# Optimization experiments

Measured on AMD Instinct MI355X. Metric: run time of the kernel, lower is better.

## Reference

```python
import jax, jax.numpy as jnp
import numpy as np

ALPHA = 0.05          # embed strength (frames in [0,1])
COEF_R, COEF_C = 4, 3 # mid-frequency DCT coefficient that carries the bit


def _dct_mat():
    # 8x8 orthonormal DCT-II matrix
    n = jnp.arange(8, dtype=jnp.float32)
    D = jnp.cos(jnp.pi * (2.0 * n[None, :] + 1.0) * n[:, None] / 16.0) * jnp.sqrt(2.0 / 8.0)
    return D.at[0].multiply(1.0 / jnp.sqrt(2.0))


def rgb_to_yuv(rgb):
    r, g, b = rgb[:, 0:1], rgb[:, 1:2], rgb[:, 2:3]
    y = 0.299 * r + 0.587 * g + 0.114 * b
    u = -0.147 * r - 0.289 * g + 0.436 * b
    v = 0.615 * r - 0.515 * g - 0.1 * b
    return jnp.concatenate([y, u, v], axis=1)


def yuv_to_rgb(yuv):
    y, u, v = yuv[:, 0:1], yuv[:, 1:2], yuv[:, 2:3]
    r = y + 1.14 * v
    g = y - 0.395 * u - 0.581 * v
    b = y + 2.032 * u
    return jnp.concatenate([r, g, b], axis=1)


def lbp_uniform(gray):
    # uniform LBP, P=8, R=1 (integer 8-neighborhood), per-image max-normalized
    B, H, W = gray.shape
    p = jnp.pad(gray, ((0, 0), (1, 1), (1, 1)), mode='edge')
    offs = [(-1, 0), (-1, 1), (0, 1), (1, 1), (1, 0), (1, -1), (0, -1), (-1, -1)]
    neigh = jnp.stack([p[:, 1 + dy:1 + dy + H, 1 + dx:1 + dx + W] for dy, dx in offs], axis=0)
    bits = (neigh >= gray[None]).astype(jnp.float32)          # [8,B,H,W]
    trans = jnp.sum(jnp.abs(bits - jnp.roll(bits, 1, axis=0)), axis=0)
    s = jnp.sum(bits, axis=0)
    code = jnp.where(trans <= 2.0, s, 9.0)
    mx = jnp.max(code, axis=(1, 2), keepdims=True)
    return code / mx                                           # [B,H,W]


def dct_embed(y, watermark, mask):
    # y: [B,H,W] luma; watermark: [L] int bits; mask: [B,H,W] texture strength
    B, H, W = y.shape
    nh, nw = H // 8, W // 8
    D = _dct_mat()
    yb = y.reshape(B, nh, 8, nw, 8).transpose(0, 1, 3, 2, 4)   # [B,nh,nw,8,8]
    coef = jnp.einsum('ij,bhwjk,lk->bhwil', D, yb, D)          # D @ block @ D^T
    strength = mask.reshape(B, nh, 8, nw, 8).mean(axis=(2, 4)) # [B,nh,nw]
    L = watermark.shape[0]
    idx = (jnp.arange(nh * nw) % L).reshape(nh, nw)
    bits = watermark[idx].astype(jnp.float32)                  # [nh,nw]
    delta = ALPHA * strength * (2.0 * bits - 1.0)[None]        # [B,nh,nw]
    coef = coef.at[..., COEF_R, COEF_C].add(delta)
    inv = jnp.einsum('ji,bhwjk,kl->bhwil', D, coef, D)         # D^T @ coef @ D
    return inv.transpose(0, 1, 3, 2, 4).reshape(B, H, W)


def _forward(frame, watermark, sa_w, sa_b, ca_w1, ca_w2):
    # LBP texture features from grayscale
    gray = 0.299 * frame[:, 0] + 0.587 * frame[:, 1] + 0.114 * frame[:, 2]
    lbp = lbp_uniform(gray)[:, None]                           # [B,1,H,W]
    # spatial attention: 7x7 conv over [frame, lbp] -> sigmoid mask
    sa_in = jnp.concatenate([frame, lbp], axis=1)
    mask = jax.nn.sigmoid(
        jax.lax.conv_general_dilated(sa_in, sa_w, (1, 1), 'SAME',
                                     dimension_numbers=('NCHW', 'OIHW', 'NCHW'))
        + sa_b[None, :, None, None])                           # [B,1,H,W]
    # channel attention on YUV
    yuv = rgb_to_yuv(frame)
    pooled = yuv.mean(axis=(2, 3))                             # [B,3]
    scale = jax.nn.sigmoid(jax.nn.relu(pooled @ ca_w1.T) @ ca_w2.T)
    weighted = yuv * scale[:, :, None, None]
    # blockwise DCT watermark embed on Y channel
    y_marked = dct_embed(weighted[:, 0], watermark, mask[:, 0])
    wm_yuv = jnp.concatenate([y_marked[:, None], weighted[:, 1:2], weighted[:, 2:3]], axis=1)
    return yuv_to_rgb(wm_yuv), mask


def setup_inputs() -> dict:
    key = jax.random.key(0)
    k1, k2, k3, k4, k5 = jax.random.split(key, 5)
    B, H, W, L = 16, 512, 512, 64
    frame = jax.random.uniform(k1, (B, 3, H, W), dtype=jnp.float32)
    watermark = jax.random.randint(k2, (L,), 0, 2, dtype=jnp.int32)
    sa_w = jax.random.normal(k3, (1, 4, 7, 7), dtype=jnp.float32) * 0.1
    sa_b = jnp.zeros((1,), dtype=jnp.float32)
    ca_w1 = jax.random.normal(k4, (3, 3), dtype=jnp.float32) * 0.5
    ca_w2 = jax.random.normal(k5, (3, 3), dtype=jnp.float32) * 0.5
    return {"frame": frame, "watermark": watermark, "sa_w": sa_w, "sa_b": sa_b,
            "ca_w1": ca_w1, "ca_w2": ca_w2}


def reference(frame, watermark, sa_w, sa_b, ca_w1, ca_w2):
    return _forward(frame, watermark, sa_w, sa_b, ca_w1, ca_w2)
```

## Files before the change

### kernel.cpp

```cpp
#include <hip/hip_runtime.h>
#include <stdint.h>

#define BB 16
#define HH 512
#define WW 512
#define HWsz (HH*WW)

__device__ __forceinline__ float grayf(float r,float g,float b){
  return __fadd_rn(__fadd_rn(__fmul_rn(0.299f,r),__fmul_rn(0.587f,g)),__fmul_rn(0.114f,b));
}
__device__ __forceinline__ float sigmoidf_(float x){ return 1.0f/(1.0f+expf(-x)); }

__device__ __forceinline__ int lbp_code(float tl,float tc,float tr,
                                        float ml,float c ,float mr,
                                        float bl,float bc,float br){
  int b0 = tc>=c, b1 = tr>=c, b2 = mr>=c, b3 = br>=c;
  int b4 = bc>=c, b5 = bl>=c, b6 = ml>=c, b7 = tl>=c;
  int s = (b0+b1)+(b2+b3)+(b4+b5)+(b6+b7);
  int tr_ = (b0!=b7)+(b1!=b0)+(b2!=b1)+(b3!=b2)+(b4!=b3)+(b5!=b4)+(b6!=b5)+(b7!=b6);
  return (tr_<=2)? s : 9;
}

__global__ void k_init(float* sums, int* maxc){
  int t = threadIdx.x;
  if(t < BB*3) sums[t] = 0.0f;
  if(t < BB) maxc[t] = 0;
}

#define RSTRIDE 520
__global__ __launch_bounds__(256,4) void k_reduce(const float* __restrict__ frame,
     float* __restrict__ sums, int* __restrict__ maxc){
  const int blk = blockIdx.x;
  const int b = blk >> 6;
  const int s = blk & 63;
  const int r0 = s*8;
  const float4* F = (const float4*)(frame + (size_t)b*3*HWsz);
  __shared__ float sg[10*RSTRIDE];
  const int tid = threadIdx.x;
  float sy=0.f, su=0.f, sv=0.f;
  #pragma unroll
  for(int k=0;k<5;k++){
    int j = tid + 256*k;
    int row = j >> 7;
    int c4  = j & 127;
    int gy  = min(max(r0-1+row,0),HH-1);
    int fi  = gy*128 + c4;
    float4 r4 = F[fi];
    float4 g4 = F[65536  + fi];
    float4 b4 = F[131072 + fi];
    float4 gr;
    gr.x = grayf(r4.x,g4.x,b4.x);
    gr.y = grayf(r4.y,g4.y,b4.y);
    gr.z = grayf(r4.z,g4.z,b4.z);
    gr.w = grayf(r4.w,g4.w,b4.w);
    *(float4*)&sg[row*RSTRIDE + 4 + 4*c4] = gr;
    if(c4==0)   sg[row*RSTRIDE + 3]   = gr.x;
    if(c4==127) sg[row*RSTRIDE + 516] = gr.w;
    if(row>=1 && row<=8){
      sy += (gr.x+gr.y)+(gr.z+gr.w);
      float rs_=(r4.x+r4.y)+(r4.z+r4.w), gs_=(g4.x+g4.y)+(g4.z+g4.w), bs_=(b4.x+b4.y)+(b4.z+b4.w);
      su += -0.147f*rs_ - 0.289f*gs_ + 0.436f*bs_;
      sv +=  0.615f*rs_ - 0.515f*gs_ - 0.1f*bs_;
    }
  }
  __syncthreads();
  int cm = 0;
  {
    const float* base = sg + (2*tid + 3);
    float t0=base[0], t1=base[1], t2=base[2], t3=base[3];
    float m0=base[RSTRIDE], m1=base[RSTRIDE+1], m2=base[RSTRIDE+2], m3=base[RSTRIDE+3];
    #pragma unroll
    for(int R=1;R<=8;R++){
      const float* brow = base + (R+1)*RSTRIDE;
      float b0=brow[0], b1=brow[1], b2=brow[2], b3=brow[3];
      cm = max(cm, lbp_code(t0,t1,t2, m0,m1,m2, b0,b1,b2));
      cm = max(cm, lbp_code(t1,t2,t3, m1,m2,m3, b1,b2,b3));
      t0=m0;t1=m1;t2=m2;t3=m3; m0=b0;m1=b1;m2=b2;m3=b3;
    }
  }
  #pragma unroll
  for(int off=32;off>=1;off>>=1){
    sy += __shfl_down(sy,off,64);
    su += __shfl_down(su,off,64);
    sv += __shfl_down(sv,off,64);
    cm = max(cm,__shfl_down(cm,off,64));
  }
  __shared__ float rs[3][4]; __shared__ int rm[4];
  int wave=tid>>6, lane=tid&63;
  if(lane==0){ rs[0][wave]=sy; rs[1][wave]=su; rs[2][wave]=sv; rm[wave]=cm; }
  __syncthreads();
  if(tid==0){
    atomicAdd(&sums[b*3+0], (rs[0][0]+rs[0][1])+(rs[0][2]+rs[0][3]));
    atomicAdd(&sums[b*3+1], (rs[1][0]+rs[1][1])+(rs[1][2]+rs[1][3]));
    atomicAdd(&sums[b*3+2], (rs[2][0]+rs[2][1])+(rs[2][2]+rs[2][3]));
    atomicMax(&maxc[b], max(max(rm[0],rm[1]),max(rm[2],rm[3])));
  }
}

__global__ void k_scale(const float* __restrict__ sums, const int* __restrict__ maxc,
    const float* __restrict__ w1, const float* __restrict__ w2,
    float* __restrict__ scale, float* __restrict__ mxf){
  int b = threadIdx.x;
  if(b >= BB) return;
  float p[3], h[3];
  for(int j=0;j<3;j++) p[j] = sums[b*3+j] * (1.0f/(float)HWsz);
  for(int i=0;i<3;i++){
    float a = p[0]*w1[i*3+0] + p[1]*w1[i*3+1] + p[2]*w1[i*3+2];
    h[i] = fmaxf(a, 0.0f);
  }
  for(int i=0;i<3;i++){
    float a = h[0]*w2[i*3+0] + h[1]*w2[i*3+1] + h[2]*w2[i*3+2];
    scale[b*3+i] = sigmoidf_(a);
  }
  mxf[b] = fmaxf((float)maxc[b], 1.0f);
}

#define SAS 41
__global__ __launch_bounds__(256,6) void k_main(const float* __restrict__ frame,
    const int* __restrict__ wm, const float* __restrict__ sa_w, const float* __restrict__ sa_b,
    const float* __restrict__ scalev, const float* __restrict__ mxf,
    float* __restrict__ out)
{
  const int b = blockIdx.z;
  const int tx0 = blockIdx.x*32, ty0 = blockIdx.y*32;
  const float* fr = frame + (size_t)b*3*HWsz;
  const float4* F4 = (const float4*)fr;

  __shared__ float sA[4][38][SAS];
  __shared__ float sgt[44];
  __shared__ float sgb[44];
  __shared__ float spart[32][8];
  __shared__ float sstr[4][4];
  __shared__ float ssc[4];
  __shared__ float scodetab[12];

  const int tid = threadIdx.x;
  if(tid < 3)  ssc[tid] = scalev[b*3 + tid];
  if(tid == 3) ssc[3] = sa_b[0];
  if(tid < 10) scodetab[tid] = (float)tid / mxf[b];

  for(int s = tid; s < 400; s += 256){
    int ly = s / 10;
    int k  = s - ly*10;
    int gy = ty0 + ly - 4;
    int ry = min(max(gy,0),HH-1);
    int gx0 = tx0 + 4*k - 4;
    bool xin = (gx0 >= 0) && (gx0 <= WW-4);
    float4 r4, g4, b4;
    if(xin){
      int fi = ry*(WW/4) + (gx0>>2);
      r4 = F4[fi]; g4 = F4[65536 + fi]; b4 = F4[131072 + fi];
    } else {
      int cc = (gx0 < 0) ? 0 : (WW-1);
      float r = fr[ry*WW+cc], g = fr[HWsz+ry*WW+cc], bl = fr[2*HWsz+ry*WW+cc];
      r4 = make_float4(r,r,r,r); g4 = make_float4(g,g,g,g); b4 = make_float4(bl,bl,bl,bl);
    }
    float gr0 = grayf(r4.x,g4.x,b4.x), gr1 = grayf(r4.y,g4.y,b4.y),
          gr2 = grayf(r4.z,g4.z,b4.z), gr3 = grayf(r4.w,g4.w,b4.w);
    int cbase = 4*k;
    float* gp = (ly==0) ? &sgt[cbase] : ((ly==39) ? &sgb[cbase] : &sA[3][ly-1][cbase]);
    gp[0]=gr0; gp[1]=gr1; gp[2]=gr2; gp[3]=gr3;
    if(ly >= 1 && ly <= 38){
      float z = ((gy >= 0) && (gy < HH) && xin) ? 1.0f : 0.0f;
      float* rp = &sA[0][ly-1][cbase];
      rp[0]          =r4.x*z; rp[1]          =r4.y*z; rp[2]          =r4.z*z; rp[3]          =r4.w*z;
      rp[38*SAS+0]   =g4.x*z; rp[38*SAS+1]   =g4.y*z; rp[38*SAS+2]   =g4.z*z; rp[38*SAS+3]   =g4.w*z;
      rp[2*38*SAS+0] =b4.x*z; rp[2*38*SAS+1] =b4.y*z; rp[2*38*SAS+2] =b4.z*z; rp[2*38*SAS+3] =b4.w*z;
    }
  }
  __syncthreads();

  float lv[2][4];
  #pragma unroll
  for(int it=0; it<2; ++it){
    int s2 = tid + 256*it;
    if(s2 < 380){
      int lr = s2 / 10;
      int q  = s2 - lr*10;
      int lx0 = 4*q;
      const float* rowM = &sA[3][lr][0];
      const float* rowT = (lr==0)  ? sgt : &sA[3][lr-1][0];
      const float* rowB = (lr==37) ? sgb : &sA[3][lr+1][0];
      float t_[6], m_[6], b_[6];
      #pragma unroll
      for(int j=0;j<6;j++){
        int c = lx0 - 1 + j;
        t_[j]=rowT[c]; m_[j]=rowM[c]; b_[j]=rowB[c];
      }
      int gy = ty0 + lr - 3;
      bool rowin = (gy >= 0) && (gy < HH);
      #pragma unroll
      for(int j=0;j<4;j++){
        int lx = lx0 + j;
        int gx = tx0 + lx - 4;
        float v = 0.0f;
        if(rowin && lx >= 1 && lx <= 38 && gx >= 0 && gx < WW){
          float c = m_[j+1];
          int msk = ((t_[j+1]>=c)?1:0)   | ((t_[j+2]>=c)?2:0)  | ((m_[j+2]>=c)?4:0) |
                    ((b_[j+2]>=c)?8:0)   | ((b_[j+1]>=c)?16:0) | ((b_[j]>=c)?32:0)  |
                    ((m_[j]>=c)?64:0)    | ((t_[j]>=c)?128:0);
          int s8  = __popc(msk);
          int rot = ((msk<<1) | (msk>>7)) & 255;
          int tr_ = __popc(msk ^ rot);
          int code = (tr_ <= 2) ? s8 : 9;
          v = scodetab[code];
        }
        lv[it][j] = v;
      }
    }
  }
  __syncthreads();
  #pragma unroll
  for(int it=0; it<2; ++it){
    int s2 = tid + 256*it;
    if(s2 < 380){
      int lr = s2 / 10;
      int q  = s2 - lr*10;
      float* wp2 = &sA[3][lr][4*q];
      wp2[0]=lv[it][0]; wp2[1]=lv[it][1]; wp2[2]=lv[it][2]; wp2[3]=lv[it][3];
    }
  }
  __syncthreads();

  const int t  = tid & 7;
  const int ty = tid >> 3;
  float a0=ssc[3], a1=ssc[3], a2=ssc[3], a3=ssc[3];
  for(int ci=0;ci<4;ci++){
    #pragma unroll
    for(int ky=0;ky<7;ky++){
      const float* rowp = &sA[ci][ty+ky][4*t];
      float win[10];
      #pragma unroll
      for(int w=0;w<10;w++) win[w]=rowp[1+w];
      const float* wr = &sa_w[ci*49 + ky*7];
      #pragma unroll
      for(int kx=0;kx<7;kx++){
        float wt = wr[kx];
        a0 += win[kx+0]*wt;
        a1 += win[kx+1]*wt;
        a2 += win[kx+2]*wt;
        a3 += win[kx+3]*wt;
      }
    }
  }
  float m0=sigmoidf_(a0), m1=sigmoidf_(a1), m2=sigmoidf_(a2), m3=sigmoidf_(a3);
  {
    size_t midx = (size_t)(3*BB)*HWsz + (size_t)b*HWsz + (size_t)(ty0+ty)*WW + (size_t)(tx0+4*t);
    *reinterpret_cast<float4*>(out + midx) = make_float4(m0,m1,m2,m3);
  }
  spart[ty][t] = (m0+m1)+(m2+m3);
  __syncthreads();

  if(tid<16){
    int rb=tid>>2, cb=tid&3;
    float ssum=0.f;
    #pragma unroll
    for(int yy=0;yy<8;yy++) ssum += spart[rb*8+yy][2*cb] + spart[rb*8+yy][2*cb+1];
    sstr[rb][cb]=ssum*(1.0f/64.0f);
  }
  __syncthreads();

  {
    const float sc0=ssc[0], sc1=ssc[1], sc2=ssc[2];
    const float strength = sstr[ty>>3][t>>1];
    const int bw = (tx0 + 4*t) >> 3;
    const float sgn = (float)(2*wm[bw]-1);
    const float d4 = (((ty+1)&2) ? -0.35355339059327373f : 0.35355339059327373f);
    const float delta = 0.05f * strength * sgn * d4;
    const float D3tab[8] = { 0.4157348061512726f,-0.0975451610080641f,-0.4903926402016152f,-0.2777851165098011f,
                             0.2777851165098011f, 0.4903926402016152f, 0.0975451610080641f,-0.4157348061512726f };
    float vr[4], vg[4], vb[4];
    #pragma unroll
    for(int j=0;j<4;j++){
      float r  = sA[0][ty+3][4*t+j+4];
      float g  = sA[1][ty+3][4*t+j+4];
      float bl = sA[2][ty+3][4*t+j+4];
      float yv = (0.299f*r + 0.587f*g + 0.114f*bl) * sc0;
      float uv = (-0.147f*r - 0.289f*g + 0.436f*bl) * sc1;
      float vv = ( 0.615f*r - 0.515f*g - 0.1f*bl) * sc2;
      float ym = yv + delta * D3tab[(t&1)*4 + j];
      vr[j] = ym + 1.14f*vv;
      vg[j] = ym - 0.395f*uv - 0.581f*vv;
      vb[j] = ym + 2.032f*uv;
    }
    size_t base = (size_t)(ty0+ty)*WW + (size_t)(tx0+4*t);
    *reinterpret_cast<float4*>(out + (size_t)(b*3+0)*HWsz + base) = make_float4(vr[0],vr[1],vr[2],vr[3]);
    *reinterpret_cast<float4*>(out + (size_t)(b*3+1)*HWsz + base) = make_float4(vg[0],vg[1],vg[2],vg[3]);
    *reinterpret_cast<float4*>(out + (size_t)(b*3+2)*HWsz + base) = make_float4(vb[0],vb[1],vb[2],vb[3]);
  }
}

extern "C" void kernel_launch(void* const* d_in, const int* in_sizes, int n_in,
                              void* d_out, int out_size, void* d_ws, size_t ws_size,
                              hipStream_t stream) {
  const float* frame = (const float*)d_in[0];
  const int*   wmark = (const int*)d_in[1];
  const float* sa_w  = (const float*)d_in[2];
  const float* sa_b  = (const float*)d_in[3];
  const float* ca_w1 = (const float*)d_in[4];
  const float* ca_w2 = (const float*)d_in[5];
  float* out = (float*)d_out;
  char* ws = (char*)d_ws;
  float* sums  = (float*)(ws);
  int*   maxc  = (int*)(ws + 192);
  float* scalev= (float*)(ws + 256);
  float* mxf   = (float*)(ws + 448);

  hipLaunchKernelGGL(k_init,  dim3(1),        dim3(64),  0, stream, sums, maxc);
  hipLaunchKernelGGL(k_reduce,dim3(1024),     dim3(256), 0, stream, frame, sums, maxc);
  hipLaunchKernelGGL(k_scale, dim3(1),        dim3(64),  0, stream, sums, maxc, ca_w1, ca_w2, scalev, mxf);
  hipLaunchKernelGGL(k_main,  dim3(16,16,16), dim3(256), 0, stream, frame, wmark, sa_w, sa_b, scalev, mxf, out);
}
```

Measured before the change: 174.7 us.

## Widen main tile to 64 columns with 8 outputs per thread and shuffle-reduce strength

Doubles the k_main tile width to 64 columns, so each thread computes eight horizontal outputs of the 7x7 attention conv and the watermark. This cuts halo reload overhead and amortises shared-memory window loads over more outputs. Each thread now covers exactly one 8-wide DCT block column, so the per-block mean strength is computed with wavefront xor-shuffles instead of a shared-memory partial array and two barriers. The trade-off is more registers and shared memory per block, with launch bounds lowered from 6 to 3 blocks per CU, which reduces occupancy.

```diff
diff --git a/kernel.cpp b/kernel.cpp
--- a/kernel.cpp
+++ b/kernel.cpp
@@ -115,22 +115,20 @@
   mxf[b] = fmaxf((float)maxc[b], 1.0f);
 }
 
-#define SAS 41
-__global__ __launch_bounds__(256,6) void k_main(const float* __restrict__ frame,
+#define SAS 73
+__global__ __launch_bounds__(256,3) void k_main(const float* __restrict__ frame,
     const int* __restrict__ wm, const float* __restrict__ sa_w, const float* __restrict__ sa_b,
     const float* __restrict__ scalev, const float* __restrict__ mxf,
     float* __restrict__ out)
 {
   const int b = blockIdx.z;
-  const int tx0 = blockIdx.x*32, ty0 = blockIdx.y*32;
+  const int tx0 = blockIdx.x*64, ty0 = blockIdx.y*32;
   const float* fr = frame + (size_t)b*3*HWsz;
   const float4* F4 = (const float4*)fr;
 
   __shared__ float sA[4][38][SAS];
-  __shared__ float sgt[44];
-  __shared__ float sgb[44];
-  __shared__ float spart[32][8];
-  __shared__ float sstr[4][4];
+  __shared__ float sgt[76];
+  __shared__ float sgb[76];
   __shared__ float ssc[4];
   __shared__ float scodetab[12];
 
@@ -139,9 +137,9 @@
   if(tid == 3) ssc[3] = sa_b[0];
   if(tid < 10) scodetab[tid] = (float)tid / mxf[b];
 
-  for(int s = tid; s < 400; s += 256){
-    int ly = s / 10;
-    int k  = s - ly*10;
+  for(int s = tid; s < 720; s += 256){
+    int ly = s / 18;
+    int k  = s - ly*18;
     int gy = ty0 + ly - 4;
     int ry = min(max(gy,0),HH-1);
     int gx0 = tx0 + 4*k - 4;
@@ -170,13 +168,13 @@
   }
   __syncthreads();
 
-  float lv[2][4];
+  float lv[3][4];
   #pragma unroll
-  for(int it=0; it<2; ++it){
+  for(int it=0; it<3; ++it){
     int s2 = tid + 256*it;
-    if(s2 < 380){
-      int lr = s2 / 10;
-      int q  = s2 - lr*10;
+    if(s2 < 684){
+      int lr = s2 / 18;
+      int q  = s2 - lr*18;
       int lx0 = 4*q;
       const float* rowM = &sA[3][lr][0];
       const float* rowT = (lr==0)  ? sgt : &sA[3][lr-1][0];
@@ -194,7 +192,7 @@
         int lx = lx0 + j;
         int gx = tx0 + lx - 4;
         float v = 0.0f;
-        if(rowin && lx >= 1 && lx <= 38 && gx >= 0 && gx < WW){
+        if(rowin && lx >= 1 && lx <= 70 && gx >= 0 && gx < WW){
           float c = m_[j+1];
           int msk = ((t_[j+1]>=c)?1:0)   | ((t_[j+2]>=c)?2:0)  | ((m_[j+2]>=c)?4:0) |
                     ((b_[j+2]>=c)?8:0)   | ((b_[j+1]>=c)?16:0) | ((b_[j]>=c)?32:0)  |
@@ -211,11 +209,11 @@
   }
   __syncthreads();
   #pragma unroll
-  for(int it=0; it<2; ++it){
+  for(int it=0; it<3; ++it){
     int s2 = tid + 256*it;
-    if(s2 < 380){
-      int lr = s2 / 10;
-      int q  = s2 - lr*10;
+    if(s2 < 684){
+      int lr = s2 / 18;
+      int q  = s2 - lr*18;
       float* wp2 = &sA[3][lr][4*q];
       wp2[0]=lv[it][0]; wp2[1]=lv[it][1]; wp2[2]=lv[it][2]; wp2[3]=lv[it][3];
     }
@@ -225,13 +223,14 @@
   const int t  = tid & 7;
   const int ty = tid >> 3;
   float a0=ssc[3], a1=ssc[3], a2=ssc[3], a3=ssc[3];
+  float a4=ssc[3], a5=ssc[3], a6=ssc[3], a7=ssc[3];
   for(int ci=0;ci<4;ci++){
     #pragma unroll
     for(int ky=0;ky<7;ky++){
-      const float* rowp = &sA[ci][ty+ky][4*t];
-      float win[10];
+      const float* rowp = &sA[ci][ty+ky][8*t];
+      float win[14];
       #pragma unroll
-      for(int w=0;w<10;w++) win[w]=rowp[1+w];
+      for(int w=0;w<14;w++) win[w]=rowp[1+w];
       const float* wr = &sa_w[ci*49 + ky*7];
       #pragma unroll
       for(int kx=0;kx<7;kx++){
@@ -240,53 +239,60 @@
         a1 += win[kx+1]*wt;
         a2 += win[kx+2]*wt;
         a3 += win[kx+3]*wt;
+        a4 += win[kx+4]*wt;
+        a5 += win[kx+5]*wt;
+        a6 += win[kx+6]*wt;
+        a7 += win[kx+7]*wt;
       }
     }
   }
-  float m0=sigmoidf_(a0), m1=sigmoidf_(a1), m2=sigmoidf_(a2), m3=sigmoidf_(a3);
+  float m[8];
+  m[0]=sigmoidf_(a0); m[1]=sigmoidf_(a1); m[2]=sigmoidf_(a2); m[3]=sigmoidf_(a3);
+  m[4]=sigmoidf_(a4); m[5]=sigmoidf_(a5); m[6]=sigmoidf_(a6); m[7]=sigmoidf_(a7);
   {
-    size_t midx = (size_t)(3*BB)*HWsz + (size_t)b*HWsz + (size_t)(ty0+ty)*WW + (size_t)(tx0+4*t);
-    *reinterpret_cast<float4*>(out + midx) = make_float4(m0,m1,m2,m3);
-  }
-  spart[ty][t] = (m0+m1)+(m2+m3);
-  __syncthreads();
-
-  if(tid<16){
-    int rb=tid>>2, cb=tid&3;
-    float ssum=0.f;
-    #pragma unroll
-    for(int yy=0;yy<8;yy++) ssum += spart[rb*8+yy][2*cb] + spart[rb*8+yy][2*cb+1];
-    sstr[rb][cb]=ssum*(1.0f/64.0f);
-  }
-  __syncthreads();
+    size_t midx = (size_t)(3*BB)*HWsz + (size_t)b*HWsz + (size_t)(ty0+ty)*WW + (size_t)(tx0+8*t);
+    *reinterpret_cast<float4*>(out + midx)     = make_float4(m[0],m[1],m[2],m[3]);
+    *reinterpret_cast<float4*>(out + midx + 4) = make_float4(m[4],m[5],m[6],m[7]);
+  }
+
+  float part = ((m[0]+m[1])+(m[2]+m[3])) + ((m[4]+m[5])+(m[6]+m[7]));
+  part += __shfl_xor(part, 8, 64);
+  part += __shfl_xor(part, 16, 64);
+  part += __shfl_xor(part, 32, 64);
+  const float strength = part * (1.0f/64.0f);
 
   {
     const float sc0=ssc[0], sc1=ssc[1], sc2=ssc[2];
-    const float strength = sstr[ty>>3][t>>1];
-    const int bw = (tx0 + 4*t) >> 3;
+    const int bw = (tx0 + 8*t) >> 3;
     const float sgn = (float)(2*wm[bw]-1);
     const float d4 = (((ty+1)&2) ? -0.35355339059327373f : 0.35355339059327373f);
     const float delta = 0.05f * strength * sgn * d4;
     const float D3tab[8] = { 0.4157348061512726f,-0.0975451610080641f,-0.4903926402016152f,-0.2777851165098011f,
                              0.2777851165098011f, 0.4903926402016152f, 0.0975451610080641f,-0.4157348061512726f };
-    float vr[4], vg[4], vb[4];
+    float vr[8], vg[8], vb[8];
     #pragma unroll
-    for(int j=0;j<4;j++){
-      float r  = sA[0][ty+3][4*t+j+4];
-      float g  = sA[1][ty+3][4*t+j+4];
-      float bl = sA[2][ty+3][4*t+j+4];
+    for(int j=0;j<8;j++){
+      float r  = sA[0][ty+3][8*t+j+4];
+      float g  = sA[1][ty+3][8*t+j+4];
+      float bl = sA[2][ty+3][8*t+j+4];
       float yv = (0.299f*r + 0.587f*g + 0.114f*bl) * sc0;
       float uv = (-0.147f*r - 0.289f*g + 0.436f*bl) * sc1;
       float vv = ( 0.615f*r - 0.515f*g - 0.1f*bl) * sc2;
-      float ym = yv + delta * D3tab[(t&1)*4 + j];
+      float ym = yv + delta * D3tab[j];
       vr[j] = ym + 1.14f*vv;
       vg[j] = ym - 0.395f*uv - 0.581f*vv;
       vb[j] = ym + 2.032f*uv;
     }
-    size_t base = (size_t)(ty0+ty)*WW + (size_t)(tx0+4*t);
-    *reinterpret_cast<float4*>(out + (size_t)(b*3+0)*HWsz + base) = make_float4(vr[0],vr[1],vr[2],vr[3]);
-    *reinterpret_cast<float4*>(out + (size_t)(b*3+1)*HWsz + base) = make_float4(vg[0],vg[1],vg[2],vg[3]);
-    *reinterpret_cast<float4*>(out + (size_t)(b*3+2)*HWsz + base) = make_float4(vb[0],vb[1],vb[2],vb[3]);
+    size_t base = (size_t)(ty0+ty)*WW + (size_t)(tx0+8*t);
+    float* o0 = out + (size_t)(b*3+0)*HWsz + base;
+    float* o1 = out + (size_t)(b*3+1)*HWsz + base;
+    float* o2 = out + (size_t)(b*3+2)*HWsz + base;
+    *reinterpret_cast<float4*>(o0)   = make_float4(vr[0],vr[1],vr[2],vr[3]);
+    *reinterpret_cast<float4*>(o0+4) = make_float4(vr[4],vr[5],vr[6],vr[7]);
+    *reinterpret_cast<float4*>(o1)   = make_float4(vg[0],vg[1],vg[2],vg[3]);
+    *reinterpret_cast<float4*>(o1+4) = make_float4(vg[4],vg[5],vg[6],vg[7]);
+    *reinterpret_cast<float4*>(o2)   = make_float4(vb[0],vb[1],vb[2],vb[3]);
+    *reinterpret_cast<float4*>(o2+4) = make_float4(vb[4],vb[5],vb[6],vb[7]);
   }
 }
 
@@ -309,5 +315,5 @@
   hipLaunchKernelGGL(k_init,  dim3(1),        dim3(64),  0, stream, sums, maxc);
   hipLaunchKernelGGL(k_reduce,dim3(1024),     dim3(256), 0, stream, frame, sums, maxc);
   hipLaunchKernelGGL(k_scale, dim3(1),        dim3(64),  0, stream, sums, maxc, ca_w1, ca_w2, scalev, mxf);
-  hipLaunchKernelGGL(k_main,  dim3(16,16,16), dim3(256), 0, stream, frame, wmark, sa_w, sa_b, scalev, mxf, out);
-}
+  hipLaunchKernelGGL(k_main,  dim3(8,16,16),  dim3(256), 0, stream, frame, wmark, sa_w, sa_b, scalev, mxf, out);
+}
```

After: 187.6 us. 7.4% more time.
